# Kernel optimization log

Hardware: AMD Instinct MI355X
Metric: run time of the kernel (lower is better)

## Reference

```python
import jax, jax.numpy as jnp
import numpy as np

BATCH = 1048576
D_IN = 4        # d_in=3 spatial dims + 1 time dim
HID = 64
N_HID_STACK = 4  # hidden residual blocks after the first hidden layer
D_OUT = 3
BN_EPS = 1e-5


def _bn(x, gamma, beta):
    # BatchNorm1d in training mode: biased batch statistics over the batch axis
    mu = jnp.mean(x, axis=0)
    var = jnp.var(x, axis=0)
    return gamma * (x - mu) * jax.lax.rsqrt(var + BN_EPS) + beta


def setup_inputs() -> dict:
    key = jax.random.key(0)
    ks = jax.random.split(key, 8)
    s_in = 1.0 / np.sqrt(D_IN)
    s_h = 1.0 / np.sqrt(HID)
    return {
        "x": jax.random.normal(ks[0], (BATCH, D_IN), dtype=jnp.float32),
        "bn0_gamma": jnp.ones((D_IN,), jnp.float32),
        "bn0_beta": jnp.zeros((D_IN,), jnp.float32),
        "W0": jax.random.normal(ks[1], (D_IN, HID), jnp.float32) * s_in,
        "b0": jnp.zeros((HID,), jnp.float32),
        "gamma0": jnp.ones((HID,), jnp.float32),
        "beta0": jnp.zeros((HID,), jnp.float32),
        "W_hid": jax.random.normal(ks[2], (N_HID_STACK, HID, HID), jnp.float32) * s_h,
        "b_hid": jnp.zeros((N_HID_STACK, HID), jnp.float32),
        "gamma_hid": jnp.ones((N_HID_STACK, HID), jnp.float32),
        "beta_hid": jnp.zeros((N_HID_STACK, HID), jnp.float32),
        "Wout": jax.random.normal(ks[3], (HID, D_OUT), jnp.float32) * s_h,
        "bout": jnp.zeros((D_OUT,), jnp.float32),
    }


def reference(x, bn0_gamma, bn0_beta, W0, b0, gamma0, beta0,
              W_hid, b_hid, gamma_hid, beta_hid, Wout, bout):
    # Net.forward (u-network, single patch, batch_normalization=True, tanh):
    #   x = bn0(x)
    #   y = bn(act(Linear0(x)))                 (first hidden layer, no skip)
    #   y = bn_i(act(Linear_i(y))) + y          (residual hidden layers)
    #   y = Linear_out(y)
    h = _bn(x, bn0_gamma, bn0_beta)
    y = _bn(jnp.tanh(h @ W0 + b0), gamma0, beta0)

    def step(y, layer):
        W, b, g, be = layer
        return _bn(jnp.tanh(y @ W + b), g, be) + y, None

    y, _ = jax.lax.scan(step, y, (W_hid, b_hid, gamma_hid, beta_hid))
    return y @ Wout + bout
```

## Files before the change

### kernel.cpp

```cpp
#include <hip/hip_runtime.h>
#include <stdint.h>


#define NROWS 1048576
#define EPS 1e-5f
#define INV_B 9.5367431640625e-07f
#define LOG2E2 2.885390081777927f
#define BIGGRID 16384

typedef __attribute__((ext_vector_type(8))) short bfrag;
typedef __attribute__((ext_vector_type(4))) float facc;
typedef __attribute__((ext_vector_type(4))) float f4v;

__device__ __forceinline__ float bf2f(short s) {
  union { unsigned u; float f; } v;
  v.u = ((unsigned)(unsigned short)s) << 16;
  return v.f;
}
__device__ __forceinline__ short f2bf(float f) {
  union { float f; unsigned u; } v;
  v.f = f;
  unsigned r = v.u + 0x7FFFu + ((v.u >> 16) & 1u);
  return (short)(r >> 16);
}
__device__ __forceinline__ float tanh_fast(float x) {
  float e = __builtin_amdgcn_exp2f(x * LOG2E2);
  return 1.f - 2.f * __builtin_amdgcn_rcpf(e + 1.f);
}

template <int W>
__global__ __launch_bounds__(256) void k_reduce(const float* __restrict__ P,
                                                float* __restrict__ S,
                                                int rows_per_blk) {
  __shared__ float red[256];
  const int tid = threadIdx.x;
  const int col = tid % W;
  const int grp = tid / W;
  const int G = 256 / W;
  size_t r0 = (size_t)blockIdx.x * rows_per_blk;
  float s = 0.f;
  for (int r = grp; r < rows_per_blk; r += G) s += P[(r0 + r) * W + col];
  red[tid] = s;
  __syncthreads();
  if (tid < W) {
    float t = 0.f;
#pragma unroll 4
    for (int g = 0; g < G; ++g) t += red[g * W + tid];
    atomicAdd(&S[tid], t);
  }
}


__global__ __launch_bounds__(256) void k_stats_x(const float* __restrict__ x,
                                                 float* __restrict__ P) {
  __shared__ float red[4][8];
  const int tid = threadIdx.x;
  const int wave = tid >> 6;
  size_t base = (size_t)blockIdx.x * 1024 + tid;
  float s[4] = {0.f, 0.f, 0.f, 0.f}, q[4] = {0.f, 0.f, 0.f, 0.f};
#pragma unroll
  for (int it = 0; it < 4; ++it) {
    f4v v = *(const f4v*)(x + (base + (size_t)it * 256) * 4);
#pragma unroll
    for (int k = 0; k < 4; ++k) { s[k] += v[k]; q[k] = fmaf(v[k], v[k], q[k]); }
  }
#pragma unroll
  for (int off = 32; off > 0; off >>= 1) {
#pragma unroll
    for (int k = 0; k < 4; ++k) {
      s[k] += __shfl_xor(s[k], off);
      q[k] += __shfl_xor(q[k], off);
    }
  }
  if ((tid & 63) == 0) {
#pragma unroll
    for (int k = 0; k < 4; ++k) { red[wave][k] = s[k]; red[wave][4 + k] = q[k]; }
  }
  __syncthreads();
  if (tid < 8)
    P[blockIdx.x * 8 + tid] =
        red[0][tid] + red[1][tid] + red[2][tid] + red[3][tid];
}

__global__ __launch_bounds__(256) void k_stats_z1(
    const float* __restrict__ x, const float* __restrict__ bn0g,
    const float* __restrict__ bn0b, const float* __restrict__ W0,
    const float* __restrict__ b0, const float* __restrict__ sx,
    float* __restrict__ P) {
  __shared__ float red[2][4][64];
  const int tid = threadIdx.x;
  const int lane = tid & 63;
  const int wave = tid >> 6;
  int gw = blockIdx.x * 4 + wave;
  float sc[4], sh[4];
#pragma unroll
  for (int k = 0; k < 4; ++k) {
    float mean = sx[k] * INV_B;
    float var = fmaf(-mean, mean, sx[4 + k] * INV_B);
    float rs = rsqrtf(var + EPS);
    sc[k] = bn0g[k] * rs;
    sh[k] = fmaf(-sc[k], mean, bn0b[k]);
  }
  float w[4];
#pragma unroll
  for (int k = 0; k < 4; ++k) w[k] = W0[k * 64 + lane];
  float bj = b0[lane];
  float s = 0.f, q = 0.f;
  size_t r0 = (size_t)gw * 256;
  for (int r = 0; r < 256; ++r) {
    f4v xv = *(const f4v*)(x + (r0 + r) * 4);
    float acc = bj;
#pragma unroll
    for (int k = 0; k < 4; ++k)
      acc = fmaf(fmaf(xv[k], sc[k], sh[k]), w[k], acc);
    float z = tanh_fast(acc);
    s += z;
    q = fmaf(z, z, q);
  }
  red[0][wave][lane] = s;
  red[1][wave][lane] = q;
  __syncthreads();
  if (tid < 128) {
    int which = tid >> 6, c = tid & 63;
    P[blockIdx.x * 128 + tid] = red[which][0][c] + red[which][1][c] +
                                red[which][2][c] + red[which][3][c];
  }
}

__global__ __launch_bounds__(256) void k_prep(const float* __restrict__ Wh,
                                              short* __restrict__ WT) {
  int idx = blockIdx.x * 256 + threadIdx.x;
  int l = idx >> 12, rem = idx & 4095, k = rem >> 6, c = rem & 63;
  WT[l * 4096 + c * 64 + k] = f2bf(Wh[l * 4096 + k * 64 + c]);
}


__global__ __launch_bounds__(128) void k_first(
    const float* __restrict__ x, const float* __restrict__ bn0g,
    const float* __restrict__ bn0b, const float* __restrict__ W0,
    const float* __restrict__ b0, const float* __restrict__ gamma0,
    const float* __restrict__ beta0, const float* __restrict__ sx,
    const float* __restrict__ s1, const short* __restrict__ WTb,
    const float* __restrict__ bb, float* __restrict__ P,
    short* __restrict__ Y) {
  __shared__ __align__(16) float lds_x[64 * 4];
  __shared__ __align__(16) short lds_y[64 * 72];
  __shared__ float lds_st[128];

  const int tid = threadIdx.x;
  const int lane = tid & 63;
  const int wave = tid >> 6;
  const int l15 = lane & 15;
  const int q = lane >> 4;
  const int wr = wave * 32;
  const size_t r0 = (size_t)blockIdx.x * 64;

  f4v xp;
  if (lane < 32) xp = *(const f4v*)(x + (r0 + wr + lane) * 4);

  lds_st[tid] = 0.f;
  float sc0[4], sh0[4];
#pragma unroll
  for (int k = 0; k < 4; ++k) {
    float mean = sx[k] * INV_B;
    float var = fmaf(-mean, mean, sx[4 + k] * INV_B);
    float rs = rsqrtf(var + EPS);
    sc0[k] = bn0g[k] * rs;
    sh0[k] = fmaf(-sc0[k], mean, bn0b[k]);
  }
  float w0c[4];
#pragma unroll
  for (int k = 0; k < 4; ++k) w0c[k] = W0[k * 64 + lane];
  float b0c = b0[lane];
  float mean1 = s1[lane] * INV_B;
  float var1 = fmaf(-mean1, mean1, s1[64 + lane] * INV_B);
  float A1c = gamma0[lane] * rsqrtf(var1 + EPS);
  float B1c = fmaf(-A1c, mean1, beta0[lane]);
  if (lane < 32) *(f4v*)&lds_x[(wr + lane) * 4] = xp;
  __syncthreads();

  for (int e = 0; e < 32; ++e) {
    int row = wr + e;
    float acc = b0c;
#pragma unroll
    for (int k = 0; k < 4; ++k)
      acc = fmaf(fmaf(lds_x[row * 4 + k], sc0[k], sh0[k]), w0c[k], acc);
    float z = tanh_fast(acc);
    lds_y[row * 72 + lane] = f2bf(fmaf(A1c, z, B1c));
  }

  bfrag af[2][2];
#pragma unroll
  for (int mt = 0; mt < 2; ++mt)
#pragma unroll
    for (int kt = 0; kt < 2; ++kt) {
      af[mt][kt] =
          *(const bfrag*)&lds_y[(wr + mt * 16 + l15) * 72 + kt * 32 + q * 8];
      *(bfrag*)(Y + (r0 + wr + mt * 16 + l15) * 64 + kt * 32 + q * 8) =
          af[mt][kt];
    }
  float bbv[4];
  bfrag bwb[4][2];
#pragma unroll
  for (int nt = 0; nt < 4; ++nt) {
    bbv[nt] = bb[nt * 16 + l15];
#pragma unroll
    for (int kt = 0; kt < 2; ++kt)
      bwb[nt][kt] =
          *(const bfrag*)(WTb + (nt * 16 + l15) * 64 + kt * 32 + q * 8);
  }
  facc acc2[2][4];
#pragma unroll
  for (int mt = 0; mt < 2; ++mt)
#pragma unroll
    for (int nt = 0; nt < 4; ++nt) {
      acc2[mt][nt][0] = bbv[nt]; acc2[mt][nt][1] = bbv[nt];
      acc2[mt][nt][2] = bbv[nt]; acc2[mt][nt][3] = bbv[nt];
    }
#pragma unroll
  for (int mt = 0; mt < 2; ++mt)
#pragma unroll
    for (int nt = 0; nt < 4; ++nt)
#pragma unroll
      for (int kt = 0; kt < 2; ++kt)
        acc2[mt][nt] = __builtin_amdgcn_mfma_f32_16x16x32_bf16(
            af[mt][kt], bwb[nt][kt], acc2[mt][nt], 0, 0, 0);
  float sAcc[4], qAcc[4];
#pragma unroll
  for (int nt = 0; nt < 4; ++nt) {
    sAcc[nt] = 0.f;
    qAcc[nt] = 0.f;
#pragma unroll
    for (int mt = 0; mt < 2; ++mt)
#pragma unroll
      for (int i = 0; i < 4; ++i) {
        float z = tanh_fast(acc2[mt][nt][i]);
        sAcc[nt] += z;
        qAcc[nt] = fmaf(z, z, qAcc[nt]);
      }
    float s = sAcc[nt], ss = qAcc[nt];
    s += __shfl_xor(s, 16); s += __shfl_xor(s, 32);
    ss += __shfl_xor(ss, 16); ss += __shfl_xor(ss, 32);
    if (q == 0) {
      atomicAdd(&lds_st[nt * 16 + l15], s);
      atomicAdd(&lds_st[64 + nt * 16 + l15], ss);
    }
  }
  __syncthreads();
  P[(size_t)blockIdx.x * 128 + tid] = lds_st[tid];
}

__global__ __launch_bounds__(128) void k_mid(
    short* __restrict__ Y, const short* __restrict__ WTa,
    const float* __restrict__ ba, const float* __restrict__ ga,
    const float* __restrict__ bea, const float* __restrict__ sa,
    const short* __restrict__ WTb, const float* __restrict__ bb,
    float* __restrict__ P) {
  __shared__ __align__(16) short lds_y[64 * 72];
  __shared__ float lds_st[128];

  const int tid = threadIdx.x;
  const int lane = tid & 63;
  const int wave = tid >> 6;
  const int l15 = lane & 15;
  const int q = lane >> 4;
  const int wr = wave * 32;
  const size_t r0 = (size_t)blockIdx.x * 64;
  const int srow = lane >> 3;
  const int sc8 = (lane & 7) * 8;

  bfrag ld[4];
  {
    const size_t g = (r0 + wr + srow) * 64 + sc8;
#pragma unroll
    for (int it = 0; it < 4; ++it)
      ld[it] = *(const bfrag*)(Y + g + (size_t)it * 8 * 64);
  }

  lds_st[tid] = 0.f;
  float Av[4], Bv[4], bav[4];
#pragma unroll
  for (int nt = 0; nt < 4; ++nt) {
    int c = nt * 16 + l15;
    float mean = sa[c] * INV_B;
    float var = fmaf(-mean, mean, sa[64 + c] * INV_B);
    float A = ga[c] * rsqrtf(var + EPS);
    Av[nt] = A;
    Bv[nt] = fmaf(-A, mean, bea[c]);
    bav[nt] = ba[c];
  }
  bfrag bwa[4][2];
#pragma unroll
  for (int nt = 0; nt < 4; ++nt)
#pragma unroll
    for (int kt = 0; kt < 2; ++kt)
      bwa[nt][kt] =
          *(const bfrag*)(WTa + (nt * 16 + l15) * 64 + kt * 32 + q * 8);

#pragma unroll
  for (int it = 0; it < 4; ++it)
    *(bfrag*)&lds_y[(wr + it * 8 + srow) * 72 + sc8] = ld[it];
  __syncthreads();

  bfrag af[2][2];
#pragma unroll
  for (int mt = 0; mt < 2; ++mt)
#pragma unroll
    for (int kt = 0; kt < 2; ++kt)
      af[mt][kt] =
          *(const bfrag*)&lds_y[(wr + mt * 16 + l15) * 72 + kt * 32 + q * 8];
  facc acc[2][4];
#pragma unroll
  for (int mt = 0; mt < 2; ++mt)
#pragma unroll
    for (int nt = 0; nt < 4; ++nt) {
      acc[mt][nt][0] = bav[nt]; acc[mt][nt][1] = bav[nt];
      acc[mt][nt][2] = bav[nt]; acc[mt][nt][3] = bav[nt];
    }
#pragma unroll
  for (int mt = 0; mt < 2; ++mt)
#pragma unroll
    for (int nt = 0; nt < 4; ++nt)
#pragma unroll
      for (int kt = 0; kt < 2; ++kt)
        acc[mt][nt] = __builtin_amdgcn_mfma_f32_16x16x32_bf16(
            af[mt][kt], bwa[nt][kt], acc[mt][nt], 0, 0, 0);

#pragma unroll
  for (int mt = 0; mt < 2; ++mt)
#pragma unroll
    for (int nt = 0; nt < 4; ++nt) {
      int c = nt * 16 + l15;
      float A = Av[nt], Bc = Bv[nt];
#pragma unroll
      for (int i = 0; i < 4; ++i) {
        int rl = wr + mt * 16 + q * 4 + i;
        float z = tanh_fast(acc[mt][nt][i]);
        float yo = bf2f(lds_y[rl * 72 + c]);
        lds_y[rl * 72 + c] = f2bf(fmaf(A, z, Bc) + yo);
      }
    }

#pragma unroll
  for (int mt = 0; mt < 2; ++mt)
#pragma unroll
    for (int kt = 0; kt < 2; ++kt) {
      af[mt][kt] =
          *(const bfrag*)&lds_y[(wr + mt * 16 + l15) * 72 + kt * 32 + q * 8];
      *(bfrag*)(Y + (r0 + wr + mt * 16 + l15) * 64 + kt * 32 + q * 8) =
          af[mt][kt];
    }
  float bbv[4];
  bfrag bwb[4][2];
#pragma unroll
  for (int nt = 0; nt < 4; ++nt) {
    bbv[nt] = bb[nt * 16 + l15];
#pragma unroll
    for (int kt = 0; kt < 2; ++kt)
      bwb[nt][kt] =
          *(const bfrag*)(WTb + (nt * 16 + l15) * 64 + kt * 32 + q * 8);
  }
#pragma unroll
  for (int mt = 0; mt < 2; ++mt)
#pragma unroll
    for (int nt = 0; nt < 4; ++nt) {
      acc[mt][nt][0] = bbv[nt]; acc[mt][nt][1] = bbv[nt];
      acc[mt][nt][2] = bbv[nt]; acc[mt][nt][3] = bbv[nt];
    }
#pragma unroll
  for (int mt = 0; mt < 2; ++mt)
#pragma unroll
    for (int nt = 0; nt < 4; ++nt)
#pragma unroll
      for (int kt = 0; kt < 2; ++kt)
        acc[mt][nt] = __builtin_amdgcn_mfma_f32_16x16x32_bf16(
            af[mt][kt], bwb[nt][kt], acc[mt][nt], 0, 0, 0);
#pragma unroll
  for (int nt = 0; nt < 4; ++nt) {
    float s = 0.f, ss = 0.f;
#pragma unroll
    for (int mt = 0; mt < 2; ++mt)
#pragma unroll
      for (int i = 0; i < 4; ++i) {
        float z = tanh_fast(acc[mt][nt][i]);
        s += z;
        ss = fmaf(z, z, ss);
      }
    s += __shfl_xor(s, 16); s += __shfl_xor(s, 32);
    ss += __shfl_xor(ss, 16); ss += __shfl_xor(ss, 32);
    if (q == 0) {
      atomicAdd(&lds_st[nt * 16 + l15], s);
      atomicAdd(&lds_st[64 + nt * 16 + l15], ss);
    }
  }
  __syncthreads();
  P[(size_t)blockIdx.x * 128 + tid] = lds_st[tid];
}

__global__ __launch_bounds__(128) void k_last(
    const short* __restrict__ Y, const short* __restrict__ WTa,
    const float* __restrict__ ba, const float* __restrict__ ga,
    const float* __restrict__ bea, const float* __restrict__ sa,
    const float* __restrict__ Wout, const float* __restrict__ bout,
    float* __restrict__ out) {
  __shared__ __align__(16) short lds_y[64 * 72];
  __shared__ float lds_wo[192];

  const int tid = threadIdx.x;
  const int lane = tid & 63;
  const int wave = tid >> 6;
  const int l15 = lane & 15;
  const int q = lane >> 4;
  const int wr = wave * 32;
  const size_t r0 = (size_t)blockIdx.x * 64;
  const int srow = lane >> 3;
  const int sc8 = (lane & 7) * 8;

  bfrag ld[4];
  {
    const size_t g = (r0 + wr + srow) * 64 + sc8;
#pragma unroll
    for (int it = 0; it < 4; ++it)
      ld[it] = *(const bfrag*)(Y + g + (size_t)it * 8 * 64);
  }

  for (int i = tid; i < 192; i += 128) lds_wo[i] = Wout[i];
  float Av[4], Bv[4], bav[4];
#pragma unroll
  for (int nt = 0; nt < 4; ++nt) {
    int c = nt * 16 + l15;
    float mean = sa[c] * INV_B;
    float var = fmaf(-mean, mean, sa[64 + c] * INV_B);
    float A = ga[c] * rsqrtf(var + EPS);
    Av[nt] = A;
    Bv[nt] = fmaf(-A, mean, bea[c]);
    bav[nt] = ba[c];
  }
  bfrag bwa[4][2];
#pragma unroll
  for (int nt = 0; nt < 4; ++nt)
#pragma unroll
    for (int kt = 0; kt < 2; ++kt)
      bwa[nt][kt] =
          *(const bfrag*)(WTa + (nt * 16 + l15) * 64 + kt * 32 + q * 8);
  float bo0 = bout[0], bo1 = bout[1], bo2 = bout[2];

#pragma unroll
  for (int it = 0; it < 4; ++it)
    *(bfrag*)&lds_y[(wr + it * 8 + srow) * 72 + sc8] = ld[it];
  __syncthreads();

  bfrag af[2][2];
#pragma unroll
  for (int mt = 0; mt < 2; ++mt)
#pragma unroll
    for (int kt = 0; kt < 2; ++kt)
      af[mt][kt] =
          *(const bfrag*)&lds_y[(wr + mt * 16 + l15) * 72 + kt * 32 + q * 8];
  facc acc[2][4];
#pragma unroll
  for (int mt = 0; mt < 2; ++mt)
#pragma unroll
    for (int nt = 0; nt < 4; ++nt) {
      acc[mt][nt][0] = bav[nt]; acc[mt][nt][1] = bav[nt];
      acc[mt][nt][2] = bav[nt]; acc[mt][nt][3] = bav[nt];
    }
#pragma unroll
  for (int mt = 0; mt < 2; ++mt)
#pragma unroll
    for (int nt = 0; nt < 4; ++nt)
#pragma unroll
      for (int kt = 0; kt < 2; ++kt)
        acc[mt][nt] = __builtin_amdgcn_mfma_f32_16x16x32_bf16(
            af[mt][kt], bwa[nt][kt], acc[mt][nt], 0, 0, 0);
#pragma unroll
  for (int mt = 0; mt < 2; ++mt)
#pragma unroll
    for (int nt = 0; nt < 4; ++nt) {
      int c = nt * 16 + l15;
      float A = Av[nt], Bc = Bv[nt];
#pragma unroll
      for (int i = 0; i < 4; ++i) {
        int rl = wr + mt * 16 + q * 4 + i;
        float z = tanh_fast(acc[mt][nt][i]);
        float yo = bf2f(lds_y[rl * 72 + c]);
        lds_y[rl * 72 + c] = f2bf(fmaf(A, z, Bc) + yo);
      }
    }

  {
    int row = wr + (lane >> 1);
    int cb = (lane & 1) * 32;
    float o0 = 0.f, o1 = 0.f, o2 = 0.f;
#pragma unroll
    for (int jc = 0; jc < 4; ++jc) {
      bfrag v = *(const bfrag*)&lds_y[row * 72 + cb + jc * 8];
#pragma unroll
      for (int j = 0; j < 8; ++j) {
        float f = bf2f(v[j]);
        int jj = cb + jc * 8 + j;
        o0 = fmaf(f, lds_wo[jj * 3 + 0], o0);
        o1 = fmaf(f, lds_wo[jj * 3 + 1], o1);
        o2 = fmaf(f, lds_wo[jj * 3 + 2], o2);
      }
    }
    o0 += __shfl_xor(o0, 1);
    o1 += __shfl_xor(o1, 1);
    o2 += __shfl_xor(o2, 1);
    if ((lane & 1) == 0) {
      size_t ro = (r0 + row) * 3;
      out[ro] = o0 + bo0;
      out[ro + 1] = o1 + bo1;
      out[ro + 2] = o2 + bo2;
    }
  }
}

extern "C" void kernel_launch(void* const* d_in, const int* in_sizes, int n_in,
                              void* d_out, int out_size, void* d_ws,
                              size_t ws_size, hipStream_t stream) {
  (void)in_sizes; (void)n_in; (void)out_size; (void)ws_size;
  const float* x = (const float*)d_in[0];
  const float* bn0g = (const float*)d_in[1];
  const float* bn0b = (const float*)d_in[2];
  const float* W0 = (const float*)d_in[3];
  const float* b0 = (const float*)d_in[4];
  const float* gamma0 = (const float*)d_in[5];
  const float* beta0 = (const float*)d_in[6];
  const float* Wh = (const float*)d_in[7];
  const float* bh = (const float*)d_in[8];
  const float* gh = (const float*)d_in[9];
  const float* beh = (const float*)d_in[10];
  const float* Wout = (const float*)d_in[11];
  const float* bout = (const float*)d_in[12];
  float* out = (float*)d_out;

  char* ws = (char*)d_ws;
  short* Y = (short*)ws;
  const size_t YB = (size_t)NROWS * 64 * 2;
  float* stats = (float*)(ws + YB);
  float* Sx = stats;
  float* S1 = stats + 8;
  float* S2 = stats + 136;
  float* S3 = stats + 264;
  float* S4 = stats + 392;
  float* S5 = stats + 520;
  short* WT = (short*)(ws + YB + 4096);
  float* P = (float*)(ws + YB + 4096 + 32768);

  hipMemsetAsync(stats, 0, 648 * sizeof(float), stream);
  k_prep<<<64, 256, 0, stream>>>(Wh, WT);
  k_stats_x<<<1024, 256, 0, stream>>>(x, P);
  k_reduce<8><<<8, 256, 0, stream>>>(P, Sx, 128);
  k_stats_z1<<<1024, 256, 0, stream>>>(x, bn0g, bn0b, W0, b0, Sx, P);
  k_reduce<128><<<8, 256, 0, stream>>>(P, S1, 128);
  k_first<<<BIGGRID, 128, 0, stream>>>(x, bn0g, bn0b, W0, b0, gamma0, beta0,
                                       Sx, S1, WT, bh, P, Y);
  k_reduce<128><<<128, 256, 0, stream>>>(P, S2, 128);
  k_mid<<<BIGGRID, 128, 0, stream>>>(Y, WT, bh, gh, beh, S2, WT + 4096,
                                     bh + 64, P);
  k_reduce<128><<<128, 256, 0, stream>>>(P, S3, 128);
  k_mid<<<BIGGRID, 128, 0, stream>>>(Y, WT + 4096, bh + 64, gh + 64, beh + 64,
                                     S3, WT + 2 * 4096, bh + 128, P);
  k_reduce<128><<<128, 256, 0, stream>>>(P, S4, 128);
  k_mid<<<BIGGRID, 128, 0, stream>>>(Y, WT + 2 * 4096, bh + 128, gh + 128,
                                     beh + 128, S4, WT + 3 * 4096, bh + 192, P);
  k_reduce<128><<<128, 256, 0, stream>>>(P, S5, 128);
  k_last<<<BIGGRID, 128, 0, stream>>>(Y, WT + 3 * 4096, bh + 192, gh + 192,
                                      beh + 192, S5, Wout, bout, out);
}
```

Baseline: 564.8 us.

## Make row-tile kernels persistent with double-buffered async global-to-LDS prefetch

Each block of k_first, k_mid and k_last now processes eight 64-row tiles instead of one, and the grid shrinks accordingly. The next tile is prefetched straight into a second LDS buffer with global_load_lds while the current tile is computed, and the buffer uses an XOR swizzle in place of padding to avoid bank conflicts. Weights and BN coefficients are loaded once per block, statistics accumulate in registers across tiles, and the LDS atomics are replaced by per-wave slots. The hand-written vmcnt waits and the lack of barriers between waves touching the shared buffers are fragile, and the smaller grid may not fill the GPU as well.

After: 884.6 us. 56.6% more time.

```diff
diff --git a/kernel.cpp b/kernel.cpp
--- a/kernel.cpp
+++ b/kernel.cpp
@@ -6,11 +6,13 @@
 #define EPS 1e-5f
 #define INV_B 9.5367431640625e-07f
 #define LOG2E2 2.885390081777927f
-#define BIGGRID 16384
+#define GRID_BIG 2048
+#define TILES 8
 
 typedef __attribute__((ext_vector_type(8))) short bfrag;
 typedef __attribute__((ext_vector_type(4))) float facc;
 typedef __attribute__((ext_vector_type(4))) float f4v;
+typedef unsigned int u32;
 
 __device__ __forceinline__ float bf2f(short s) {
   union { unsigned u; float f; } v;
@@ -26,6 +28,16 @@
 __device__ __forceinline__ float tanh_fast(float x) {
   float e = __builtin_amdgcn_exp2f(x * LOG2E2);
   return 1.f - 2.f * __builtin_amdgcn_rcpf(e + 1.f);
+}
+
+__device__ __forceinline__ void gld16(const void* g, void* l) {
+  __builtin_amdgcn_global_load_lds(
+      (const __attribute__((address_space(1))) u32*)g,
+      (__attribute__((address_space(3))) u32*)l, 16, 0, 0);
+}
+
+__device__ __forceinline__ int ysw(int r, int c) {
+  return (r << 6) + ((((c >> 3) ^ (r & 7)) << 3) | (c & 7));
 }
 
 template <int W>
@@ -135,7 +147,7 @@
 }
 
 
-__global__ __launch_bounds__(128) void k_first(
+__global__ __launch_bounds__(128, 3) void k_first(
     const float* __restrict__ x, const float* __restrict__ bn0g,
     const float* __restrict__ bn0b, const float* __restrict__ W0,
     const float* __restrict__ b0, const float* __restrict__ gamma0,
@@ -143,9 +155,9 @@
     const float* __restrict__ s1, const short* __restrict__ WTb,
     const float* __restrict__ bb, float* __restrict__ P,
     short* __restrict__ Y) {
-  __shared__ __align__(16) float lds_x[64 * 4];
-  __shared__ __align__(16) short lds_y[64 * 72];
-  __shared__ float lds_st[128];
+  __shared__ __align__(16) short yb[64 * 64];
+  __shared__ __align__(16) float xb[2][64 * 4];
+  __shared__ float red[256];
 
   const int tid = threadIdx.x;
   const int lane = tid & 63;
@@ -153,12 +165,10 @@
   const int l15 = lane & 15;
   const int q = lane >> 4;
   const int wr = wave * 32;
-  const size_t r0 = (size_t)blockIdx.x * 64;
-
-  f4v xp;
-  if (lane < 32) xp = *(const f4v*)(x + (r0 + wr + lane) * 4);
-
-  lds_st[tid] = 0.f;
+  const size_t row0 = (size_t)blockIdx.x * (TILES * 64);
+
+  if (lane < 32) gld16(x + (row0 + wr + lane) * 4, &xb[0][wr * 4]);
+
   float sc0[4], sh0[4];
 #pragma unroll
   for (int k = 0; k < 4; ++k) {
@@ -176,29 +186,6 @@
   float var1 = fmaf(-mean1, mean1, s1[64 + lane] * INV_B);
   float A1c = gamma0[lane] * rsqrtf(var1 + EPS);
   float B1c = fmaf(-A1c, mean1, beta0[lane]);
-  if (lane < 32) *(f4v*)&lds_x[(wr + lane) * 4] = xp;
-  __syncthreads();
-
-  for (int e = 0; e < 32; ++e) {
-    int row = wr + e;
-    float acc = b0c;
-#pragma unroll
-    for (int k = 0; k < 4; ++k)
-      acc = fmaf(fmaf(lds_x[row * 4 + k], sc0[k], sh0[k]), w0c[k], acc);
-    float z = tanh_fast(acc);
-    lds_y[row * 72 + lane] = f2bf(fmaf(A1c, z, B1c));
-  }
-
-  bfrag af[2][2];
-#pragma unroll
-  for (int mt = 0; mt < 2; ++mt)
-#pragma unroll
-    for (int kt = 0; kt < 2; ++kt) {
-      af[mt][kt] =
-          *(const bfrag*)&lds_y[(wr + mt * 16 + l15) * 72 + kt * 32 + q * 8];
-      *(bfrag*)(Y + (r0 + wr + mt * 16 + l15) * 64 + kt * 32 + q * 8) =
-          af[mt][kt];
-    }
   float bbv[4];
   bfrag bwb[4][2];
 #pragma unroll
@@ -209,55 +196,93 @@
       bwb[nt][kt] =
           *(const bfrag*)(WTb + (nt * 16 + l15) * 64 + kt * 32 + q * 8);
   }
-  facc acc2[2][4];
-#pragma unroll
-  for (int mt = 0; mt < 2; ++mt)
-#pragma unroll
-    for (int nt = 0; nt < 4; ++nt) {
-      acc2[mt][nt][0] = bbv[nt]; acc2[mt][nt][1] = bbv[nt];
-      acc2[mt][nt][2] = bbv[nt]; acc2[mt][nt][3] = bbv[nt];
-    }
-#pragma unroll
-  for (int mt = 0; mt < 2; ++mt)
+  float sA[4] = {0.f, 0.f, 0.f, 0.f}, qA[4] = {0.f, 0.f, 0.f, 0.f};
+
+#pragma unroll 1
+  for (int t = 0; t < TILES; ++t) {
+    const size_t r0 = row0 + (size_t)t * 64;
+    const float* xcur = xb[t & 1];
+    if (t < TILES - 1) {
+      if (lane < 32)
+        gld16(x + (r0 + 64 + wr + lane) * 4, &xb[(t & 1) ^ 1][wr * 4]);
+      if (t == 0)
+        asm volatile("s_waitcnt vmcnt(1)" ::: "memory");
+      else
+        asm volatile("s_waitcnt vmcnt(5)" ::: "memory");
+    } else {
+      asm volatile("s_waitcnt vmcnt(4)" ::: "memory");
+    }
+
+    for (int e = 0; e < 32; ++e) {
+      int row = wr + e;
+      float accv = b0c;
+#pragma unroll
+      for (int k = 0; k < 4; ++k)
+        accv = fmaf(fmaf(xcur[row * 4 + k], sc0[k], sh0[k]), w0c[k], accv);
+      float z = tanh_fast(accv);
+      yb[ysw(row, lane)] = f2bf(fmaf(A1c, z, B1c));
+    }
+
+    bfrag af[2][2];
+#pragma unroll
+    for (int mt = 0; mt < 2; ++mt)
+#pragma unroll
+      for (int kt = 0; kt < 2; ++kt) {
+        af[mt][kt] = *(const bfrag*)&yb[ysw(wr + mt * 16 + l15,
+                                            kt * 32 + q * 8)];
+        *(bfrag*)(Y + (r0 + wr + mt * 16 + l15) * 64 + kt * 32 + q * 8) =
+            af[mt][kt];
+      }
+    facc acc2[2][4];
+#pragma unroll
+    for (int mt = 0; mt < 2; ++mt)
+#pragma unroll
+      for (int nt = 0; nt < 4; ++nt) {
+        acc2[mt][nt][0] = bbv[nt]; acc2[mt][nt][1] = bbv[nt];
+        acc2[mt][nt][2] = bbv[nt]; acc2[mt][nt][3] = bbv[nt];
+      }
+#pragma unroll
+    for (int mt = 0; mt < 2; ++mt)
+#pragma unroll
+      for (int nt = 0; nt < 4; ++nt)
+#pragma unroll
+        for (int kt = 0; kt < 2; ++kt)
+          acc2[mt][nt] = __builtin_amdgcn_mfma_f32_16x16x32_bf16(
+              af[mt][kt], bwb[nt][kt], acc2[mt][nt], 0, 0, 0);
 #pragma unroll
     for (int nt = 0; nt < 4; ++nt)
 #pragma unroll
-      for (int kt = 0; kt < 2; ++kt)
-        acc2[mt][nt] = __builtin_amdgcn_mfma_f32_16x16x32_bf16(
-            af[mt][kt], bwb[nt][kt], acc2[mt][nt], 0, 0, 0);
-  float sAcc[4], qAcc[4];
+      for (int mt = 0; mt < 2; ++mt)
+#pragma unroll
+        for (int i = 0; i < 4; ++i) {
+          float z = tanh_fast(acc2[mt][nt][i]);
+          sA[nt] += z;
+          qA[nt] = fmaf(z, z, qA[nt]);
+        }
+  }
+
 #pragma unroll
   for (int nt = 0; nt < 4; ++nt) {
-    sAcc[nt] = 0.f;
-    qAcc[nt] = 0.f;
-#pragma unroll
-    for (int mt = 0; mt < 2; ++mt)
-#pragma unroll
-      for (int i = 0; i < 4; ++i) {
-        float z = tanh_fast(acc2[mt][nt][i]);
-        sAcc[nt] += z;
-        qAcc[nt] = fmaf(z, z, qAcc[nt]);
-      }
-    float s = sAcc[nt], ss = qAcc[nt];
+    float s = sA[nt], ss = qA[nt];
     s += __shfl_xor(s, 16); s += __shfl_xor(s, 32);
     ss += __shfl_xor(ss, 16); ss += __shfl_xor(ss, 32);
     if (q == 0) {
-      atomicAdd(&lds_st[nt * 16 + l15], s);
-      atomicAdd(&lds_st[64 + nt * 16 + l15], ss);
+      red[wave * 128 + nt * 16 + l15] = s;
+      red[wave * 128 + 64 + nt * 16 + l15] = ss;
     }
   }
   __syncthreads();
-  P[(size_t)blockIdx.x * 128 + tid] = lds_st[tid];
-}
-
-__global__ __launch_bounds__(128) void k_mid(
+  P[(size_t)blockIdx.x * 128 + tid] = red[tid] + red[128 + tid];
+}
+
+__global__ __launch_bounds__(128, 3) void k_mid(
     short* __restrict__ Y, const short* __restrict__ WTa,
     const float* __restrict__ ba, const float* __restrict__ ga,
     const float* __restrict__ bea, const float* __restrict__ sa,
     const short* __restrict__ WTb, const float* __restrict__ bb,
     float* __restrict__ P) {
-  __shared__ __align__(16) short lds_y[64 * 72];
-  __shared__ float lds_st[128];
+  __shared__ __align__(16) short yb[2][64 * 64];
+  __shared__ float red[256];
 
   const int tid = threadIdx.x;
   const int lane = tid & 63;
@@ -265,20 +290,16 @@
   const int l15 = lane & 15;
   const int q = lane >> 4;
   const int wr = wave * 32;
-  const size_t r0 = (size_t)blockIdx.x * 64;
-  const int srow = lane >> 3;
-  const int sc8 = (lane & 7) * 8;
-
-  bfrag ld[4];
-  {
-    const size_t g = (r0 + wr + srow) * 64 + sc8;
-#pragma unroll
-    for (int it = 0; it < 4; ++it)
-      ld[it] = *(const bfrag*)(Y + g + (size_t)it * 8 * 64);
-  }
-
-  lds_st[tid] = 0.f;
-  float Av[4], Bv[4], bav[4];
+  const size_t row0 = (size_t)blockIdx.x * (TILES * 64);
+
+#pragma unroll
+  for (int j = 0; j < 4; ++j) {
+    int rl = wr + j * 8 + (lane >> 3);
+    int cu = ((lane & 7) ^ (rl & 7)) * 8;
+    gld16(Y + (row0 + rl) * 64 + cu, &yb[0][(wr + j * 8) * 64]);
+  }
+
+  float Av[4], Bv[4], bav[4], bbv[4];
 #pragma unroll
   for (int nt = 0; nt < 4; ++nt) {
     int c = nt * 16 + l15;
@@ -288,122 +309,137 @@
     Av[nt] = A;
     Bv[nt] = fmaf(-A, mean, bea[c]);
     bav[nt] = ba[c];
-  }
-  bfrag bwa[4][2];
+    bbv[nt] = bb[c];
+  }
+  bfrag bwa[4][2], bwb[4][2];
 #pragma unroll
   for (int nt = 0; nt < 4; ++nt)
 #pragma unroll
-    for (int kt = 0; kt < 2; ++kt)
+    for (int kt = 0; kt < 2; ++kt) {
       bwa[nt][kt] =
           *(const bfrag*)(WTa + (nt * 16 + l15) * 64 + kt * 32 + q * 8);
-
-#pragma unroll
-  for (int it = 0; it < 4; ++it)
-    *(bfrag*)&lds_y[(wr + it * 8 + srow) * 72 + sc8] = ld[it];
-  __syncthreads();
-
-  bfrag af[2][2];
-#pragma unroll
-  for (int mt = 0; mt < 2; ++mt)
-#pragma unroll
-    for (int kt = 0; kt < 2; ++kt)
-      af[mt][kt] =
-          *(const bfrag*)&lds_y[(wr + mt * 16 + l15) * 72 + kt * 32 + q * 8];
-  facc acc[2][4];
-#pragma unroll
-  for (int mt = 0; mt < 2; ++mt)
-#pragma unroll
-    for (int nt = 0; nt < 4; ++nt) {
-      acc[mt][nt][0] = bav[nt]; acc[mt][nt][1] = bav[nt];
-      acc[mt][nt][2] = bav[nt]; acc[mt][nt][3] = bav[nt];
-    }
-#pragma unroll
-  for (int mt = 0; mt < 2; ++mt)
-#pragma unroll
-    for (int nt = 0; nt < 4; ++nt)
-#pragma unroll
-      for (int kt = 0; kt < 2; ++kt)
-        acc[mt][nt] = __builtin_amdgcn_mfma_f32_16x16x32_bf16(
-            af[mt][kt], bwa[nt][kt], acc[mt][nt], 0, 0, 0);
-
-#pragma unroll
-  for (int mt = 0; mt < 2; ++mt)
-#pragma unroll
-    for (int nt = 0; nt < 4; ++nt) {
-      int c = nt * 16 + l15;
-      float A = Av[nt], Bc = Bv[nt];
-#pragma unroll
-      for (int i = 0; i < 4; ++i) {
-        int rl = wr + mt * 16 + q * 4 + i;
-        float z = tanh_fast(acc[mt][nt][i]);
-        float yo = bf2f(lds_y[rl * 72 + c]);
-        lds_y[rl * 72 + c] = f2bf(fmaf(A, z, Bc) + yo);
-      }
-    }
-
-#pragma unroll
-  for (int mt = 0; mt < 2; ++mt)
-#pragma unroll
-    for (int kt = 0; kt < 2; ++kt) {
-      af[mt][kt] =
-          *(const bfrag*)&lds_y[(wr + mt * 16 + l15) * 72 + kt * 32 + q * 8];
-      *(bfrag*)(Y + (r0 + wr + mt * 16 + l15) * 64 + kt * 32 + q * 8) =
-          af[mt][kt];
-    }
-  float bbv[4];
-  bfrag bwb[4][2];
-#pragma unroll
-  for (int nt = 0; nt < 4; ++nt) {
-    bbv[nt] = bb[nt * 16 + l15];
-#pragma unroll
-    for (int kt = 0; kt < 2; ++kt)
       bwb[nt][kt] =
           *(const bfrag*)(WTb + (nt * 16 + l15) * 64 + kt * 32 + q * 8);
-  }
-#pragma unroll
-  for (int mt = 0; mt < 2; ++mt)
-#pragma unroll
-    for (int nt = 0; nt < 4; ++nt) {
-      acc[mt][nt][0] = bbv[nt]; acc[mt][nt][1] = bbv[nt];
-      acc[mt][nt][2] = bbv[nt]; acc[mt][nt][3] = bbv[nt];
-    }
-#pragma unroll
-  for (int mt = 0; mt < 2; ++mt)
+    }
+  float sA[4] = {0.f, 0.f, 0.f, 0.f}, qA[4] = {0.f, 0.f, 0.f, 0.f};
+
+#pragma unroll 1
+  for (int t = 0; t < TILES; ++t) {
+    const size_t r0 = row0 + (size_t)t * 64;
+    short* cur = &yb[t & 1][0];
+    if (t < TILES - 1) {
+      short* nxt = &yb[(t & 1) ^ 1][0];
+#pragma unroll
+      for (int j = 0; j < 4; ++j) {
+        int rl = wr + j * 8 + (lane >> 3);
+        int cu = ((lane & 7) ^ (rl & 7)) * 8;
+        gld16(Y + (r0 + 64 + rl) * 64 + cu, nxt + (wr + j * 8) * 64);
+      }
+      if (t == 0)
+        asm volatile("s_waitcnt vmcnt(4)" ::: "memory");
+      else
+        asm volatile("s_waitcnt vmcnt(8)" ::: "memory");
+    } else {
+      asm volatile("s_waitcnt vmcnt(4)" ::: "memory");
+    }
+
+    bfrag af[2][2];
+#pragma unroll
+    for (int mt = 0; mt < 2; ++mt)
+#pragma unroll
+      for (int kt = 0; kt < 2; ++kt)
+        af[mt][kt] = *(const bfrag*)&cur[ysw(wr + mt * 16 + l15,
+                                             kt * 32 + q * 8)];
+    facc acc[2][4];
+#pragma unroll
+    for (int mt = 0; mt < 2; ++mt)
+#pragma unroll
+      for (int nt = 0; nt < 4; ++nt) {
+        acc[mt][nt][0] = bav[nt]; acc[mt][nt][1] = bav[nt];
+        acc[mt][nt][2] = bav[nt]; acc[mt][nt][3] = bav[nt];
+      }
+#pragma unroll
+    for (int mt = 0; mt < 2; ++mt)
+#pragma unroll
+      for (int nt = 0; nt < 4; ++nt)
+#pragma unroll
+        for (int kt = 0; kt < 2; ++kt)
+          acc[mt][nt] = __builtin_amdgcn_mfma_f32_16x16x32_bf16(
+              af[mt][kt], bwa[nt][kt], acc[mt][nt], 0, 0, 0);
+
+#pragma unroll
+    for (int mt = 0; mt < 2; ++mt)
+#pragma unroll
+      for (int nt = 0; nt < 4; ++nt) {
+        int c = nt * 16 + l15;
+        float A = Av[nt], Bc = Bv[nt];
+#pragma unroll
+        for (int i = 0; i < 4; ++i) {
+          int rl = wr + mt * 16 + q * 4 + i;
+          int ad = ysw(rl, c);
+          float z = tanh_fast(acc[mt][nt][i]);
+          float yo = bf2f(cur[ad]);
+          cur[ad] = f2bf(fmaf(A, z, Bc) + yo);
+        }
+      }
+
+#pragma unroll
+    for (int mt = 0; mt < 2; ++mt)
+#pragma unroll
+      for (int kt = 0; kt < 2; ++kt) {
+        af[mt][kt] = *(const bfrag*)&cur[ysw(wr + mt * 16 + l15,
+                                             kt * 32 + q * 8)];
+        *(bfrag*)(Y + (r0 + wr + mt * 16 + l15) * 64 + kt * 32 + q * 8) =
+            af[mt][kt];
+      }
+#pragma unroll
+    for (int mt = 0; mt < 2; ++mt)
+#pragma unroll
+      for (int nt = 0; nt < 4; ++nt) {
+        acc[mt][nt][0] = bbv[nt]; acc[mt][nt][1] = bbv[nt];
+        acc[mt][nt][2] = bbv[nt]; acc[mt][nt][3] = bbv[nt];
+      }
+#pragma unroll
+    for (int mt = 0; mt < 2; ++mt)
+#pragma unroll
+      for (int nt = 0; nt < 4; ++nt)
+#pragma unroll
+        for (int kt = 0; kt < 2; ++kt)
+          acc[mt][nt] = __builtin_amdgcn_mfma_f32_16x16x32_bf16(
+              af[mt][kt], bwb[nt][kt], acc[mt][nt], 0, 0, 0);
 #pragma unroll
     for (int nt = 0; nt < 4; ++nt)
 #pragma unroll
-      for (int kt = 0; kt < 2; ++kt)
-        acc[mt][nt] = __builtin_amdgcn_mfma_f32_16x16x32_bf16(
-            af[mt][kt], bwb[nt][kt], acc[mt][nt], 0, 0, 0);
+      for (int mt = 0; mt < 2; ++mt)
+#pragma unroll
+        for (int i = 0; i < 4; ++i) {
+          float z = tanh_fast(acc[mt][nt][i]);
+          sA[nt] += z;
+          qA[nt] = fmaf(z, z, qA[nt]);
+        }
+  }
+
 #pragma unroll
   for (int nt = 0; nt < 4; ++nt) {
-    float s = 0.f, ss = 0.f;
-#pragma unroll
-    for (int mt = 0; mt < 2; ++mt)
-#pragma unroll
-      for (int i = 0; i < 4; ++i) {
-        float z = tanh_fast(acc[mt][nt][i]);
-        s += z;
-        ss = fmaf(z, z, ss);
-      }
+    float s = sA[nt], ss = qA[nt];
     s += __shfl_xor(s, 16); s += __shfl_xor(s, 32);
     ss += __shfl_xor(ss, 16); ss += __shfl_xor(ss, 32);
     if (q == 0) {
-      atomicAdd(&lds_st[nt * 16 + l15], s);
-      atomicAdd(&lds_st[64 + nt * 16 + l15], ss);
+      red[wave * 128 + nt * 16 + l15] = s;
+      red[wave * 128 + 64 + nt * 16 + l15] = ss;
     }
   }
   __syncthreads();
-  P[(size_t)blockIdx.x * 128 + tid] = lds_st[tid];
-}
-
-__global__ __launch_bounds__(128) void k_last(
+  P[(size_t)blockIdx.x * 128 + tid] = red[tid] + red[128 + tid];
+}
+
+__global__ __launch_bounds__(128, 3) void k_last(
     const short* __restrict__ Y, const short* __restrict__ WTa,
     const float* __restrict__ ba, const float* __restrict__ ga,
     const float* __restrict__ bea, const float* __restrict__ sa,
     const float* __restrict__ Wout, const float* __restrict__ bout,
     float* __restrict__ out) {
-  __shared__ __align__(16) short lds_y[64 * 72];
+  __shared__ __align__(16) short yb[2][64 * 64];
   __shared__ float lds_wo[192];
 
   const int tid = threadIdx.x;
@@ -412,16 +448,13 @@
   const int l15 = lane & 15;
   const int q = lane >> 4;
   const int wr = wave * 32;
-  const size_t r0 = (size_t)blockIdx.x * 64;
-  const int srow = lane >> 3;
-  const int sc8 = (lane & 7) * 8;
-
-  bfrag ld[4];
-  {
-    const size_t g = (r0 + wr + srow) * 64 + sc8;
-#pragma unroll
-    for (int it = 0; it < 4; ++it)
-      ld[it] = *(const bfrag*)(Y + g + (size_t)it * 8 * 64);
+  const size_t row0 = (size_t)blockIdx.x * (TILES * 64);
+
+#pragma unroll
+  for (int j = 0; j < 4; ++j) {
+    int rl = wr + j * 8 + (lane >> 3);
+    int cu = ((lane & 7) ^ (rl & 7)) * 8;
+    gld16(Y + (row0 + rl) * 64 + cu, &yb[0][(wr + j * 8) * 64]);
   }
 
   for (int i = tid; i < 192; i += 128) lds_wo[i] = Wout[i];
@@ -444,74 +477,89 @@
       bwa[nt][kt] =
           *(const bfrag*)(WTa + (nt * 16 + l15) * 64 + kt * 32 + q * 8);
   float bo0 = bout[0], bo1 = bout[1], bo2 = bout[2];
-
-#pragma unroll
-  for (int it = 0; it < 4; ++it)
-    *(bfrag*)&lds_y[(wr + it * 8 + srow) * 72 + sc8] = ld[it];
   __syncthreads();
 
-  bfrag af[2][2];
-#pragma unroll
-  for (int mt = 0; mt < 2; ++mt)
-#pragma unroll
-    for (int kt = 0; kt < 2; ++kt)
-      af[mt][kt] =
-          *(const bfrag*)&lds_y[(wr + mt * 16 + l15) * 72 + kt * 32 + q * 8];
-  facc acc[2][4];
-#pragma unroll
-  for (int mt = 0; mt < 2; ++mt)
-#pragma unroll
-    for (int nt = 0; nt < 4; ++nt) {
-      acc[mt][nt][0] = bav[nt]; acc[mt][nt][1] = bav[nt];
-      acc[mt][nt][2] = bav[nt]; acc[mt][nt][3] = bav[nt];
-    }
-#pragma unroll
-  for (int mt = 0; mt < 2; ++mt)
-#pragma unroll
-    for (int nt = 0; nt < 4; ++nt)
+#pragma unroll 1
+  for (int t = 0; t < TILES; ++t) {
+    const size_t r0 = row0 + (size_t)t * 64;
+    short* cur = &yb[t & 1][0];
+    if (t < TILES - 1) {
+      short* nxt = &yb[(t & 1) ^ 1][0];
+#pragma unroll
+      for (int j = 0; j < 4; ++j) {
+        int rl = wr + j * 8 + (lane >> 3);
+        int cu = ((lane & 7) ^ (rl & 7)) * 8;
+        gld16(Y + (r0 + 64 + rl) * 64 + cu, nxt + (wr + j * 8) * 64);
+      }
+      asm volatile("s_waitcnt vmcnt(4)" ::: "memory");
+    } else {
+      asm volatile("s_waitcnt vmcnt(0)" ::: "memory");
+    }
+
+    bfrag af[2][2];
+#pragma unroll
+    for (int mt = 0; mt < 2; ++mt)
 #pragma unroll
       for (int kt = 0; kt < 2; ++kt)
-        acc[mt][nt] = __builtin_amdgcn_mfma_f32_16x16x32_bf16(
-            af[mt][kt], bwa[nt][kt], acc[mt][nt], 0, 0, 0);
-#pragma unroll
-  for (int mt = 0; mt < 2; ++mt)
-#pragma unroll
-    for (int nt = 0; nt < 4; ++nt) {
-      int c = nt * 16 + l15;
-      float A = Av[nt], Bc = Bv[nt];
-#pragma unroll
-      for (int i = 0; i < 4; ++i) {
-        int rl = wr + mt * 16 + q * 4 + i;
-        float z = tanh_fast(acc[mt][nt][i]);
-        float yo = bf2f(lds_y[rl * 72 + c]);
-        lds_y[rl * 72 + c] = f2bf(fmaf(A, z, Bc) + yo);
-      }
-    }
-
-  {
-    int row = wr + (lane >> 1);
-    int cb = (lane & 1) * 32;
-    float o0 = 0.f, o1 = 0.f, o2 = 0.f;
-#pragma unroll
-    for (int jc = 0; jc < 4; ++jc) {
-      bfrag v = *(const bfrag*)&lds_y[row * 72 + cb + jc * 8];
-#pragma unroll
-      for (int j = 0; j < 8; ++j) {
-        float f = bf2f(v[j]);
-        int jj = cb + jc * 8 + j;
-        o0 = fmaf(f, lds_wo[jj * 3 + 0], o0);
-        o1 = fmaf(f, lds_wo[jj * 3 + 1], o1);
-        o2 = fmaf(f, lds_wo[jj * 3 + 2], o2);
-      }
-    }
-    o0 += __shfl_xor(o0, 1);
-    o1 += __shfl_xor(o1, 1);
-    o2 += __shfl_xor(o2, 1);
-    if ((lane & 1) == 0) {
-      size_t ro = (r0 + row) * 3;
-      out[ro] = o0 + bo0;
-      out[ro + 1] = o1 + bo1;
-      out[ro + 2] = o2 + bo2;
+        af[mt][kt] = *(const bfrag*)&cur[ysw(wr + mt * 16 + l15,
+                                             kt * 32 + q * 8)];
+    facc acc[2][4];
+#pragma unroll
+    for (int mt = 0; mt < 2; ++mt)
+#pragma unroll
+      for (int nt = 0; nt < 4; ++nt) {
+        acc[mt][nt][0] = bav[nt]; acc[mt][nt][1] = bav[nt];
+        acc[mt][nt][2] = bav[nt]; acc[mt][nt][3] = bav[nt];
+      }
+#pragma unroll
+    for (int mt = 0; mt < 2; ++mt)
+#pragma unroll
+      for (int nt = 0; nt < 4; ++nt)
+#pragma unroll
+        for (int kt = 0; kt < 2; ++kt)
+          acc[mt][nt] = __builtin_amdgcn_mfma_f32_16x16x32_bf16(
+              af[mt][kt], bwa[nt][kt], acc[mt][nt], 0, 0, 0);
+#pragma unroll
+    for (int mt = 0; mt < 2; ++mt)
+#pragma unroll
+      for (int nt = 0; nt < 4; ++nt) {
+        int c = nt * 16 + l15;
+        float A = Av[nt], Bc = Bv[nt];
+#pragma unroll
+        for (int i = 0; i < 4; ++i) {
+          int rl = wr + mt * 16 + q * 4 + i;
+          int ad = ysw(rl, c);
+          float z = tanh_fast(acc[mt][nt][i]);
+          float yo = bf2f(cur[ad]);
+          cur[ad] = f2bf(fmaf(A, z, Bc) + yo);
+        }
+      }
+
+    {
+      int row = wr + (lane >> 1);
+      int cb = (lane & 1) * 32;
+      float o0 = 0.f, o1 = 0.f, o2 = 0.f;
+#pragma unroll
+      for (int jc = 0; jc < 4; ++jc) {
+        bfrag v = *(const bfrag*)&cur[ysw(row, cb + jc * 8)];
+#pragma unroll
+        for (int j = 0; j < 8; ++j) {
+          float f = bf2f(v[j]);
+          int jj = cb + jc * 8 + j;
+          o0 = fmaf(f, lds_wo[jj * 3 + 0], o0);
+          o1 = fmaf(f, lds_wo[jj * 3 + 1], o1);
+          o2 = fmaf(f, lds_wo[jj * 3 + 2], o2);
+        }
+      }
+      o0 += __shfl_xor(o0, 1);
+      o1 += __shfl_xor(o1, 1);
+      o2 += __shfl_xor(o2, 1);
+      if ((lane & 1) == 0) {
+        size_t ro = (r0 + row) * 3;
+        out[ro] = o0 + bo0;
+        out[ro + 1] = o1 + bo1;
+        out[ro + 2] = o2 + bo2;
+      }
     }
   }
 }
@@ -554,18 +602,19 @@
   k_reduce<8><<<8, 256, 0, stream>>>(P, Sx, 128);
   k_stats_z1<<<1024, 256, 0, stream>>>(x, bn0g, bn0b, W0, b0, Sx, P);
   k_reduce<128><<<8, 256, 0, stream>>>(P, S1, 128);
-  k_first<<<BIGGRID, 128, 0, stream>>>(x, bn0g, bn0b, W0, b0, gamma0, beta0,
-                                       Sx, S1, WT, bh, P, Y);
-  k_reduce<128><<<128, 256, 0, stream>>>(P, S2, 128);
-  k_mid<<<BIGGRID, 128, 0, stream>>>(Y, WT, bh, gh, beh, S2, WT + 4096,
-                                     bh + 64, P);
-  k_reduce<128><<<128, 256, 0, stream>>>(P, S3, 128);
-  k_mid<<<BIGGRID, 128, 0, stream>>>(Y, WT + 4096, bh + 64, gh + 64, beh + 64,
-                                     S3, WT + 2 * 4096, bh + 128, P);
-  k_reduce<128><<<128, 256, 0, stream>>>(P, S4, 128);
-  k_mid<<<BIGGRID, 128, 0, stream>>>(Y, WT + 2 * 4096, bh + 128, gh + 128,
-                                     beh + 128, S4, WT + 3 * 4096, bh + 192, P);
-  k_reduce<128><<<128, 256, 0, stream>>>(P, S5, 128);
-  k_last<<<BIGGRID, 128, 0, stream>>>(Y, WT + 3 * 4096, bh + 192, gh + 192,
-                                      beh + 192, S5, Wout, bout, out);
-}
+  k_first<<<GRID_BIG, 128, 0, stream>>>(x, bn0g, bn0b, W0, b0, gamma0, beta0,
+                                        Sx, S1, WT, bh, P, Y);
+  k_reduce<128><<<16, 256, 0, stream>>>(P, S2, 128);
+  k_mid<<<GRID_BIG, 128, 0, stream>>>(Y, WT, bh, gh, beh, S2, WT + 4096,
+                                      bh + 64, P);
+  k_reduce<128><<<16, 256, 0, stream>>>(P, S3, 128);
+  k_mid<<<GRID_BIG, 128, 0, stream>>>(Y, WT + 4096, bh + 64, gh + 64, beh + 64,
+                                      S3, WT + 2 * 4096, bh + 128, P);
+  k_reduce<128><<<16, 256, 0, stream>>>(P, S4, 128);
+  k_mid<<<GRID_BIG, 128, 0, stream>>>(Y, WT + 2 * 4096, bh + 128, gh + 128,
+                                      beh + 128, S4, WT + 3 * 4096, bh + 192,
+                                      P);
+  k_reduce<128><<<16, 256, 0, stream>>>(P, S5, 128);
+  k_last<<<GRID_BIG, 128, 0, stream>>>(Y, WT + 3 * 4096, bh + 192, gh + 192,
+                                       beh + 192, S5, Wout, bout, out);
+}
```
